# Optimization experiments

Hardware: AMD Instinct MI355X
Metric: run time of the kernel (lower is better)

Reference implementation:

```python
import jax, jax.numpy as jnp
import numpy as np
import math

B, L, DIM = 2, 2048, 2048
N_HEADS, N_KV = 16, 4
HD = DIM // N_HEADS          # 128
N_REP = N_HEADS // N_KV      # 4
THETA = 10000.0


def setup_inputs() -> dict:
    key = jax.random.key(0)
    ks = jax.random.split(key, 6)
    x = jax.random.normal(ks[0], (B, L, DIM), dtype=jnp.float32)
    # rotary phasor freqs_cis = exp(i * t * inv_freq), stored as cos/sin
    inv_freq = 1.0 / (THETA ** (jnp.arange(0, HD, 2, dtype=jnp.float32) / HD))  # [HD//2]
    ang = jnp.arange(L, dtype=jnp.float32)[:, None] * inv_freq[None, :]          # [L, HD//2]
    freqs_cos = jnp.cos(ang)
    freqs_sin = jnp.sin(ang)
    s = 0.02
    wq = jax.random.normal(ks[1], (DIM, DIM), dtype=jnp.float32) * s
    wk = jax.random.normal(ks[2], (N_KV * HD, DIM), dtype=jnp.float32) * s
    wv = jax.random.normal(ks[3], (N_KV * HD, DIM), dtype=jnp.float32) * s
    wo = jax.random.normal(ks[4], (DIM, DIM), dtype=jnp.float32) * s
    return {"x": x, "freqs_cos": freqs_cos, "freqs_sin": freqs_sin,
            "wq": wq, "wk": wk, "wv": wv, "wo": wo}


def _apply_rope(t, cos, sin):
    # t: [B, L, H, HD]; cos/sin: [L, HD//2] -> broadcast [1, L, 1, HD//2]
    tr = t.reshape(*t.shape[:-1], HD // 2, 2)
    t0, t1 = tr[..., 0], tr[..., 1]
    c = cos[None, :, None, :]
    s = sin[None, :, None, :]
    r0 = t0 * c - t1 * s
    r1 = t0 * s + t1 * c
    return jnp.stack([r0, r1], axis=-1).reshape(t.shape)


def reference(x, freqs_cos, freqs_sin, wq, wk, wv, wo):
    Bx, Lx, _ = x.shape
    xq = (x @ wq.T).reshape(Bx, Lx, N_HEADS, HD)
    xk = (x @ wk.T).reshape(Bx, Lx, N_KV, HD)
    xv = (x @ wv.T).reshape(Bx, Lx, N_KV, HD)
    xq = _apply_rope(xq, freqs_cos, freqs_sin)
    xk = _apply_rope(xk, freqs_cos, freqs_sin)
    # repeat_kv (GQA expansion) then [B, H, L, HD]
    keys = jnp.repeat(xk, N_REP, axis=2).transpose(0, 2, 1, 3)
    values = jnp.repeat(xv, N_REP, axis=2).transpose(0, 2, 1, 3)
    q = xq.transpose(0, 2, 1, 3)
    scores = jnp.einsum('bhqd,bhkd->bhqk', q, keys) / math.sqrt(HD)
    mask = jnp.triu(jnp.full((Lx, Lx), -jnp.inf, dtype=scores.dtype), k=1)
    scores = scores + mask[None, None]
    probs = jax.nn.softmax(scores.astype(jnp.float32), axis=-1).astype(q.dtype)
    out = jnp.einsum('bhqk,bhkd->bhqd', probs, values)
    out = out.transpose(0, 2, 1, 3).reshape(Bx, Lx, -1)
    output = out @ wo.T
    return (output, keys, values)
```

## Files before the change

kernel.cpp:

```cpp
#include <hip/hip_runtime.h>
#include <hip/hip_bf16.h>

using bf16x8 = __attribute__((ext_vector_type(8))) short;
using f32x4  = __attribute__((ext_vector_type(4))) float;

__device__ __forceinline__ unsigned short f32_to_bf16(float f) {
  unsigned u = __float_as_uint(f);
  u += 0x7FFFu + ((u >> 16) & 1u);
  return (unsigned short)(u >> 16);
}
__device__ __forceinline__ unsigned pack2(float lo, float hi) {
  __hip_bfloat162 h = __float22bfloat162_rn(make_float2(lo, hi));
  return *reinterpret_cast<unsigned*>(&h);
}
__device__ __forceinline__ void gload_lds16(const void* g, void* l) {
  __builtin_amdgcn_global_load_lds(
      (const __attribute__((address_space(1))) unsigned int*)g,
      (__attribute__((address_space(3))) unsigned int*)l, 16, 0, 0);
}

__global__ void cast_all_kernel(const float* __restrict__ wq, const float* __restrict__ wo,
                                const float* __restrict__ wk, const float* __restrict__ wv,
                                const float* __restrict__ x,
                                unsigned short* __restrict__ WQKV,
                                unsigned short* __restrict__ WO,
                                unsigned short* __restrict__ XBF) {
  int i = blockIdx.x * blockDim.x + threadIdx.x;
  const float4* s; ushort4* d; int j;
  if (i < 1048576)      { s = (const float4*)wq; d = (ushort4*)WQKV;            j = i; }
  else if (i < 2097152) { s = (const float4*)wo; d = (ushort4*)WO;              j = i - 1048576; }
  else if (i < 2359296) { s = (const float4*)wk; d = (ushort4*)WQKV + 1048576;  j = i - 2097152; }
  else if (i < 2621440) { s = (const float4*)wv; d = (ushort4*)WQKV + 1310720;  j = i - 2359296; }
  else                  { s = (const float4*)x;  d = (ushort4*)XBF;             j = i - 2621440; }
  float4 v = s[j];
  ushort4 o;
  o.x = f32_to_bf16(v.x); o.y = f32_to_bf16(v.y);
  o.z = f32_to_bf16(v.z); o.w = f32_to_bf16(v.w);
  d[j] = o;
}

template <int BM>
__global__ __launch_bounds__(512, 2) void gemm256_kernel(
    const unsigned short* __restrict__ A, const unsigned short* __restrict__ Bw,
    float* __restrict__ C, int M, int N, int K) {
  constexpr int ABYTES = BM * 128;
  constexpr int BBYTES = 256 * 128;
  constexpr int BUFB   = ABYTES + BBYTES;
  constexpr int ALOADS = BM / 64;
  constexpr int WROWS  = BM / 32;
  __shared__ __align__(16) char Lsh[2 * BUFB];

  const int tid = threadIdx.x;
  const int wid = tid >> 6, lane = tid & 63;
  const int lr = lane & 15, lg = lane >> 4;
  const int wr = wid >> 2, wc = wid & 3;
  const int bn = blockIdx.x, bm = blockIdx.y;
  const int x0 = lg * 16;

  f32x4 acc[WROWS][4] = {};

  const char* Ag = (const char*)A + (size_t)(bm * BM) * K * 2;
  const char* Bg = (const char*)Bw + (size_t)(bn * 256) * K * 2;

  int aoff[ALOADS], boff[4];
#pragma unroll
  for (int i = 0; i < ALOADS; ++i) {
    int lin = wid * (BM * 16) + i * 1024 + lane * 16;
    int grow = lin >> 7;
    int gcol = (lin & 127) ^ ((grow & 7) << 4);
    aoff[i] = grow * (K * 2) + gcol;
  }
#pragma unroll
  for (int i = 0; i < 4; ++i) {
    int lin = wid * 4096 + i * 1024 + lane * 16;
    int grow = lin >> 7;
    int gcol = (lin & 127) ^ ((grow & 7) << 4);
    boff[i] = grow * (K * 2) + gcol;
  }

  auto stage = [&](int s, int buf) {
    const int kb = s * 128;
    char* Lb = Lsh + buf * BUFB;
#pragma unroll
    for (int i = 0; i < ALOADS; ++i)
      gload_lds16(Ag + aoff[i] + kb, Lb + wid * (BM * 16) + i * 1024);
#pragma unroll
    for (int i = 0; i < 4; ++i)
      gload_lds16(Bg + boff[i] + kb, Lb + ABYTES + wid * 4096 + i * 1024);
  };

  auto kstep = [&](char* Lb) {
    bf16x8 bfr[4][2];
#pragma unroll
    for (int fc = 0; fc < 4; ++fc) {
      const int row = wc * 64 + fc * 16 + lr;
      const int base = ABYTES + row * 128;
      const int sw = (row & 7) << 4;
#pragma unroll
      for (int ks = 0; ks < 2; ++ks)
        bfr[fc][ks] = *reinterpret_cast<const bf16x8*>(Lb + base + ((ks * 64 + x0) ^ sw));
    }
#pragma unroll
    for (int q = 0; q < WROWS / 2; ++q) {
      bf16x8 af[2][2];
#pragma unroll
      for (int t = 0; t < 2; ++t) {
        const int row = wr * (BM / 2) + (2 * q + t) * 16 + lr;
        const int base = row * 128;
        const int sw = (row & 7) << 4;
#pragma unroll
        for (int ks = 0; ks < 2; ++ks)
          af[t][ks] = *reinterpret_cast<const bf16x8*>(Lb + base + ((ks * 64 + x0) ^ sw));
      }
      asm volatile("s_waitcnt lgkmcnt(0)" ::: "memory");
      __builtin_amdgcn_sched_barrier(0);
      __builtin_amdgcn_s_setprio(1);
#pragma unroll
      for (int t = 0; t < 2; ++t)
#pragma unroll
        for (int fc = 0; fc < 4; ++fc) {
          acc[2 * q + t][fc] = __builtin_amdgcn_mfma_f32_16x16x32_bf16(af[t][0], bfr[fc][0], acc[2 * q + t][fc], 0, 0, 0);
          acc[2 * q + t][fc] = __builtin_amdgcn_mfma_f32_16x16x32_bf16(af[t][1], bfr[fc][1], acc[2 * q + t][fc], 0, 0, 0);
        }
      __builtin_amdgcn_s_setprio(0);
    }
  };

  const int NST = K >> 6;
  stage(0, 0);
  for (int it = 0; it < NST / 2; ++it) {
    __builtin_amdgcn_s_barrier();
    stage(2 * it + 1, 1);
    if constexpr (BM == 256) asm volatile("s_waitcnt vmcnt(8)" ::: "memory");
    else                     asm volatile("s_waitcnt vmcnt(6)" ::: "memory");
    __builtin_amdgcn_s_barrier();
    kstep(Lsh);
    __builtin_amdgcn_s_barrier();
    if (it < NST / 2 - 1) {
      stage(2 * it + 2, 0);
      if constexpr (BM == 256) asm volatile("s_waitcnt vmcnt(8)" ::: "memory");
      else                     asm volatile("s_waitcnt vmcnt(6)" ::: "memory");
    } else {
      asm volatile("s_waitcnt vmcnt(0)" ::: "memory");
    }
    __builtin_amdgcn_s_barrier();
    kstep(Lsh + BUFB);
  }

#pragma unroll
  for (int fr = 0; fr < WROWS; ++fr) {
    const int m = bm * BM + wr * (BM / 2) + fr * 16 + lg * 4;
#pragma unroll
    for (int fc = 0; fc < 4; ++fc) {
      const int n = bn * 256 + wc * 64 + fc * 16 + lr;
#pragma unroll
      for (int r = 0; r < 4; ++r)
        C[(size_t)(m + r) * N + n] = acc[fr][fc][r];
    }
  }
}

__global__ void kv_proc_kernel(const float* __restrict__ xqkv, const float* __restrict__ fc,
                               const float* __restrict__ fs, unsigned short* __restrict__ kbf,
                               float* __restrict__ keys, unsigned short* __restrict__ vt,
                               float* __restrict__ values) {
  int bid = blockIdx.x;
  if (bid < 4096) {
    int idx = bid * 256 + threadIdx.x;
    int i = idx & 63;
    int kvh = (idx >> 6) & 3;
    int l = (idx >> 8) & 2047;
    int b = idx >> 19;
    float2 t = reinterpret_cast<const float2*>(xqkv)[(size_t)(b * 2048 + l) * 1536 + 1024 + kvh * 64 + i];
    float c = fc[l * 64 + i], s = fs[l * 64 + i];
    float r0 = t.x * c - t.y * s;
    float r1 = t.x * s + t.y * c;
    int kidx = ((b * 4 + kvh) * 2048 + l) * 64 + i;
    ushort2 o; o.x = f32_to_bf16(r0); o.y = f32_to_bf16(r1);
    reinterpret_cast<ushort2*>(kbf)[kidx] = o;
    float2 f; f.x = r0; f.y = r1;
#pragma unroll
    for (int rep = 0; rep < 4; ++rep) {
      int h = kvh * 4 + rep;
      reinterpret_cast<float2*>(keys)[((b * 16 + h) * 2048 + l) * 64 + i] = f;
    }
  } else {
    int idx = (bid - 4096) * 256 + threadIdx.x;
    int d = idx & 127;
    int kvh = (idx >> 7) & 3;
    int l = (idx >> 9) & 2047;
    int b = idx >> 20;
    float v = xqkv[(size_t)(b * 2048 + l) * 3072 + 2560 + kvh * 128 + d];
#pragma unroll
    for (int rep = 0; rep < 4; ++rep) {
      int h = kvh * 4 + rep;
      values[((size_t)(b * 16 + h) * 2048 + l) * 128 + d] = v;
    }
    vt[((size_t)(b * 4 + kvh) * 128 + d) * 2048 + l] = f32_to_bf16(v);
  }
}

__global__ __launch_bounds__(256) void attn_kernel(
    const float* __restrict__ xq, const float* __restrict__ fc,
    const float* __restrict__ fs, const unsigned short* __restrict__ kbf,
    const unsigned short* __restrict__ vt, unsigned short* __restrict__ obf) {
  __shared__ unsigned short Ks[64 * 128];
  __shared__ unsigned short Vs[128 * 64];
  __shared__ unsigned short Ps[4][2][16 * 72];
  const int tid = threadIdx.x;
  const int w = tid >> 6, lane = tid & 63;
  const int lr = lane & 15, lg = lane >> 4;
  const int bid = blockIdx.x;
  const int qt = 15 - (bid >> 5);
  const int bh = bid & 31;
  const int b = bh >> 4, h = bh & 15, kv = h >> 2;
  const int q0 = qt * 128 + w * 32;
  const float ALPHA = 0.08838834764831845f;
  const int swz = (lr & 7) << 4;

  bf16x8 qf[2][4];
#pragma unroll
  for (int t = 0; t < 2; ++t) {
    const int qrow = q0 + t * 16 + lr;
    const float* xqp = xq + (size_t)(b * 2048 + qrow) * 3072 + h * 128;
    const float* fcp = fc + qrow * 64;
    const float* fsp = fs + qrow * 64;
#pragma unroll
    for (int s = 0; s < 4; ++s) {
      float4 f0 = *reinterpret_cast<const float4*>(xqp + s * 32 + lg * 8);
      float4 f1 = *reinterpret_cast<const float4*>(xqp + s * 32 + lg * 8 + 4);
      float4 c4 = *reinterpret_cast<const float4*>(fcp + s * 16 + lg * 4);
      float4 s4 = *reinterpret_cast<const float4*>(fsp + s * 16 + lg * 4);
      c4.x *= ALPHA; c4.y *= ALPHA; c4.z *= ALPHA; c4.w *= ALPHA;
      s4.x *= ALPHA; s4.y *= ALPHA; s4.z *= ALPHA; s4.w *= ALPHA;
      union { bf16x8 v8; unsigned u[4]; } uu;
      uu.u[0] = pack2(f0.x * c4.x - f0.y * s4.x, f0.x * s4.x + f0.y * c4.x);
      uu.u[1] = pack2(f0.z * c4.y - f0.w * s4.y, f0.z * s4.y + f0.w * c4.y);
      uu.u[2] = pack2(f1.x * c4.z - f1.y * s4.z, f1.x * s4.z + f1.y * c4.z);
      uu.u[3] = pack2(f1.z * c4.w - f1.w * s4.w, f1.z * s4.w + f1.w * c4.w);
      qf[t][s] = uu.v8;
    }
  }

  f32x4 acc[2][8] = {};
  float mrow[2] = {-1e30f, -1e30f}, lsum[2] = {0.f, 0.f};

  const char* kgbase = (const char*)(kbf + (size_t)(b * 4 + kv) * 2048 * 128);
  const char* vgbase = (const char*)(vt + (size_t)(b * 4 + kv) * 128 * 2048);

  const int nblocks = 2 * qt + 2;
  for (int j = 0; j < nblocks; ++j) {
    const int kb = j * 64;
    __syncthreads();
#pragma unroll
    for (int i = 0; i < 4; ++i) {
      int p = w * 4096 + i * 1024 + lane * 16;
      int krow = p >> 8;
      int kcol = (p & 255) ^ ((krow & 7) << 4);
      gload_lds16(kgbase + (size_t)(kb + krow) * 256 + kcol, (char*)Ks + w * 4096 + i * 1024);
      int drow = p >> 7;
      int dcol = (p & 127) ^ ((drow & 7) << 4);
      gload_lds16(vgbase + (size_t)drow * 4096 + (size_t)kb * 2 + dcol, (char*)Vs + w * 4096 + i * 1024);
    }
    __syncthreads();
    if (j == nblocks - 1 && w < 2) continue;
    f32x4 sT[2][4];
#pragma unroll
    for (int c = 0; c < 4; ++c) {
      bf16x8 kf[4];
#pragma unroll
      for (int s = 0; s < 4; ++s)
        kf[s] = *reinterpret_cast<const bf16x8*>((char*)Ks + (((c * 16 + lr) * 256 + s * 64 + lg * 16) ^ swz));
      f32x4 t0 = {0.f, 0.f, 0.f, 0.f}, t1 = {0.f, 0.f, 0.f, 0.f};
#pragma unroll
      for (int s = 0; s < 4; ++s) {
        t0 = __builtin_amdgcn_mfma_f32_16x16x32_bf16(kf[s], qf[0][s], t0, 0, 0, 0);
        t1 = __builtin_amdgcn_mfma_f32_16x16x32_bf16(kf[s], qf[1][s], t1, 0, 0, 0);
      }
      sT[0][c] = t0; sT[1][c] = t1;
    }
#pragma unroll
    for (int t = 0; t < 2; ++t) {
      const int qrow = q0 + t * 16 + lr;
      float x[4][4];
      float mt = -1e30f;
#pragma unroll
      for (int c = 0; c < 4; ++c)
#pragma unroll
        for (int r = 0; r < 4; ++r) {
          int k = kb + c * 16 + lg * 4 + r;
          float v = (k <= qrow) ? sT[t][c][r] : -1e30f;
          x[c][r] = v;
          mt = fmaxf(mt, v);
        }
      mt = fmaxf(mt, __shfl_xor(mt, 16));
      mt = fmaxf(mt, __shfl_xor(mt, 32));
      const bool skip = __all(mt <= mrow[t] + 8.0f);
      float mnew, fac;
      if (skip) {
        mnew = mrow[t];
      } else {
        mnew = fmaxf(mrow[t], mt);
        fac = __expf(mrow[t] - mnew);
        mrow[t] = mnew;
      }
      float rs = 0.f;
      unsigned pw[4][2];
#pragma unroll
      for (int c = 0; c < 4; ++c)
#pragma unroll
        for (int j2 = 0; j2 < 2; ++j2) {
          float p0 = __expf(x[c][2 * j2] - mnew);
          float p1 = __expf(x[c][2 * j2 + 1] - mnew);
          rs += p0 + p1;
          pw[c][j2] = pack2(p0, p1);
        }
      rs += __shfl_xor(rs, 16);
      rs += __shfl_xor(rs, 32);
      if (skip) {
        lsum[t] += rs;
      } else {
        lsum[t] = lsum[t] * fac + rs;
#pragma unroll
        for (int dt = 0; dt < 8; ++dt)
#pragma unroll
          for (int r = 0; r < 4; ++r) acc[t][dt][r] *= fac;
      }
      char* pb = (char*)&Ps[w][t][0];
#pragma unroll
      for (int c = 0; c < 4; ++c)
#pragma unroll
        for (int j2 = 0; j2 < 2; ++j2)
          *reinterpret_cast<unsigned*>(pb + lr * 144 + c * 32 + lg * 8 + j2 * 4) = pw[c][j2];
    }
    asm volatile("s_waitcnt lgkmcnt(0)" ::: "memory");
    __builtin_amdgcn_sched_barrier(0);
    bf16x8 pt[2][2];
#pragma unroll
    for (int t = 0; t < 2; ++t)
#pragma unroll
      for (int kk = 0; kk < 2; ++kk)
        pt[t][kk] = *reinterpret_cast<const bf16x8*>((char*)&Ps[w][t][0] + lr * 144 + kk * 64 + lg * 16);
#pragma unroll
    for (int dt = 0; dt < 8; ++dt) {
      bf16x8 v0 = *reinterpret_cast<const bf16x8*>((char*)Vs + (((dt * 16 + lr) * 128 + lg * 16) ^ swz));
      bf16x8 v1 = *reinterpret_cast<const bf16x8*>((char*)Vs + (((dt * 16 + lr) * 128 + 64 + lg * 16) ^ swz));
      acc[0][dt] = __builtin_amdgcn_mfma_f32_16x16x32_bf16(v0, pt[0][0], acc[0][dt], 0, 0, 0);
      acc[0][dt] = __builtin_amdgcn_mfma_f32_16x16x32_bf16(v1, pt[0][1], acc[0][dt], 0, 0, 0);
      acc[1][dt] = __builtin_amdgcn_mfma_f32_16x16x32_bf16(v0, pt[1][0], acc[1][dt], 0, 0, 0);
      acc[1][dt] = __builtin_amdgcn_mfma_f32_16x16x32_bf16(v1, pt[1][1], acc[1][dt], 0, 0, 0);
    }
  }
#pragma unroll
  for (int t = 0; t < 2; ++t) {
    float inv = 1.0f / lsum[t];
#pragma unroll
    for (int dt = 0; dt < 8; ++dt) {
      ushort4 o;
      o.x = f32_to_bf16(acc[t][dt][0] * inv);
      o.y = f32_to_bf16(acc[t][dt][1] * inv);
      o.z = f32_to_bf16(acc[t][dt][2] * inv);
      o.w = f32_to_bf16(acc[t][dt][3] * inv);
      *reinterpret_cast<ushort4*>(obf + ((size_t)(b * 2048 + q0 + t * 16 + lr)) * 2048 + h * 128 + dt * 16 + lg * 4) = o;
    }
  }
}

extern "C" void kernel_launch(void* const* d_in, const int* in_sizes, int n_in,
                              void* d_out, int out_size, void* d_ws, size_t ws_size,
                              hipStream_t stream) {
  const float* x  = (const float*)d_in[0];
  const float* fc = (const float*)d_in[1];
  const float* fs = (const float*)d_in[2];
  const float* wq = (const float*)d_in[3];
  const float* wk = (const float*)d_in[4];
  const float* wv = (const float*)d_in[5];
  const float* wo = (const float*)d_in[6];

  float* out    = (float*)d_out;
  float* keys   = out + 8388608;
  float* values = out + 16777216;

  char* ws = (char*)d_ws;
  unsigned short* WQKV = (unsigned short*)(ws + 0);
  unsigned short* WO   = (unsigned short*)(ws + 12582912);
  unsigned short* XBF  = (unsigned short*)(ws + 20971520);
  float*          XQKV = (float*)(ws + 37748736);
  unsigned short* KBF  = (unsigned short*)(ws + 88080384);
  unsigned short* VTB  = (unsigned short*)(ws + 92274688);
  unsigned short* ATT  = XBF;

  cast_all_kernel<<<18432, 256, 0, stream>>>(wq, wo, wk, wv, x, WQKV, WO, XBF);

  gemm256_kernel<128><<<dim3(12, 32), 512, 0, stream>>>(XBF, WQKV, XQKV, 4096, 3072, 2048);

  kv_proc_kernel<<<12288, 256, 0, stream>>>(XQKV, fc, fs, KBF, keys, VTB, values);

  attn_kernel<<<512, 256, 0, stream>>>(XQKV, fc, fs, KBF, VTB, ATT);

  gemm256_kernel<128><<<dim3(8, 32), 512, 0, stream>>>(ATT, WO, out, 4096, 2048, 2048);
}
```

Measured before the change: 234.0 us.

## Emit Q projection as bf16 and split KV output; use BM=256 for QKV GEMM

The QKV GEMM epilogue now writes the Q part directly as bf16 into a dense buffer and the K/V part as fp32 into a separate compact buffer, instead of one fp32 XQKV matrix. The attention kernel reads bf16 Q and widens it before applying RoPE, and kv_proc uses the new compact layout. The aim is less epilogue write traffic and less Q read traffic. The QKV GEMM also switches to a 256-row tile with half the blocks in M. Q is now rounded to bf16 before RoPE, which adds a second rounding step.

```diff
diff --git a/kernel.cpp b/kernel.cpp
--- a/kernel.cpp
+++ b/kernel.cpp
@@ -39,10 +39,11 @@
   d[j] = o;
 }
 
-template <int BM>
+template <int BM, int MODE>
 __global__ __launch_bounds__(512, 2) void gemm256_kernel(
     const unsigned short* __restrict__ A, const unsigned short* __restrict__ Bw,
-    float* __restrict__ C, int M, int N, int K) {
+    float* __restrict__ C, unsigned short* __restrict__ qbf_out,
+    float* __restrict__ xkv_out, int M, int N, int K) {
   constexpr int ABYTES = BM * 128;
   constexpr int BBYTES = 256 * 128;
   constexpr int BUFB   = ABYTES + BBYTES;
@@ -147,20 +148,48 @@
     kstep(Lsh + BUFB);
   }
 
-#pragma unroll
-  for (int fr = 0; fr < WROWS; ++fr) {
-    const int m = bm * BM + wr * (BM / 2) + fr * 16 + lg * 4;
-#pragma unroll
-    for (int fc = 0; fc < 4; ++fc) {
-      const int n = bn * 256 + wc * 64 + fc * 16 + lr;
-#pragma unroll
-      for (int r = 0; r < 4; ++r)
-        C[(size_t)(m + r) * N + n] = acc[fr][fc][r];
-    }
-  }
-}
-
-__global__ void kv_proc_kernel(const float* __restrict__ xqkv, const float* __restrict__ fc,
+  if constexpr (MODE == 0) {
+#pragma unroll
+    for (int fr = 0; fr < WROWS; ++fr) {
+      const int m = bm * BM + wr * (BM / 2) + fr * 16 + lg * 4;
+#pragma unroll
+      for (int fc = 0; fc < 4; ++fc) {
+        const int n = bn * 256 + wc * 64 + fc * 16 + lr;
+#pragma unroll
+        for (int r = 0; r < 4; ++r)
+          C[(size_t)(m + r) * N + n] = acc[fr][fc][r];
+      }
+    }
+  } else {
+    if (bn < 8) {
+#pragma unroll
+      for (int fr = 0; fr < WROWS; ++fr) {
+        const int m = bm * BM + wr * (BM / 2) + fr * 16 + lg * 4;
+#pragma unroll
+        for (int fc = 0; fc < 4; ++fc) {
+          const int n = bn * 256 + wc * 64 + fc * 16 + lr;
+#pragma unroll
+          for (int r = 0; r < 4; ++r)
+            qbf_out[(size_t)(m + r) * 2048 + n] = f32_to_bf16(acc[fr][fc][r]);
+        }
+      }
+    } else {
+#pragma unroll
+      for (int fr = 0; fr < WROWS; ++fr) {
+        const int m = bm * BM + wr * (BM / 2) + fr * 16 + lg * 4;
+#pragma unroll
+        for (int fc = 0; fc < 4; ++fc) {
+          const int n = bn * 256 + wc * 64 + fc * 16 + lr - 2048;
+#pragma unroll
+          for (int r = 0; r < 4; ++r)
+            xkv_out[(size_t)(m + r) * 1024 + n] = acc[fr][fc][r];
+        }
+      }
+    }
+  }
+}
+
+__global__ void kv_proc_kernel(const float* __restrict__ xkv, const float* __restrict__ fc,
                                const float* __restrict__ fs, unsigned short* __restrict__ kbf,
                                float* __restrict__ keys, unsigned short* __restrict__ vt,
                                float* __restrict__ values) {
@@ -171,7 +200,7 @@
     int kvh = (idx >> 6) & 3;
     int l = (idx >> 8) & 2047;
     int b = idx >> 19;
-    float2 t = reinterpret_cast<const float2*>(xqkv)[(size_t)(b * 2048 + l) * 1536 + 1024 + kvh * 64 + i];
+    float2 t = reinterpret_cast<const float2*>(xkv)[(size_t)(b * 2048 + l) * 512 + kvh * 64 + i];
     float c = fc[l * 64 + i], s = fs[l * 64 + i];
     float r0 = t.x * c - t.y * s;
     float r1 = t.x * s + t.y * c;
@@ -190,7 +219,7 @@
     int kvh = (idx >> 7) & 3;
     int l = (idx >> 9) & 2047;
     int b = idx >> 20;
-    float v = xqkv[(size_t)(b * 2048 + l) * 3072 + 2560 + kvh * 128 + d];
+    float v = xkv[(size_t)(b * 2048 + l) * 1024 + 512 + kvh * 128 + d];
 #pragma unroll
     for (int rep = 0; rep < 4; ++rep) {
       int h = kvh * 4 + rep;
@@ -201,7 +230,7 @@
 }
 
 __global__ __launch_bounds__(256) void attn_kernel(
-    const float* __restrict__ xq, const float* __restrict__ fc,
+    const unsigned short* __restrict__ qbf, const float* __restrict__ fc,
     const float* __restrict__ fs, const unsigned short* __restrict__ kbf,
     const unsigned short* __restrict__ vt, unsigned short* __restrict__ obf) {
   __shared__ unsigned short Ks[64 * 128];
@@ -222,22 +251,25 @@
 #pragma unroll
   for (int t = 0; t < 2; ++t) {
     const int qrow = q0 + t * 16 + lr;
-    const float* xqp = xq + (size_t)(b * 2048 + qrow) * 3072 + h * 128;
+    const unsigned short* xqp = qbf + (size_t)(b * 2048 + qrow) * 2048 + h * 128;
     const float* fcp = fc + qrow * 64;
     const float* fsp = fs + qrow * 64;
 #pragma unroll
     for (int s = 0; s < 4; ++s) {
-      float4 f0 = *reinterpret_cast<const float4*>(xqp + s * 32 + lg * 8);
-      float4 f1 = *reinterpret_cast<const float4*>(xqp + s * 32 + lg * 8 + 4);
+      union { bf16x8 v8; unsigned short us[8]; } rw;
+      rw.v8 = *reinterpret_cast<const bf16x8*>(xqp + s * 32 + lg * 8);
+      float xv[8];
+#pragma unroll
+      for (int k = 0; k < 8; ++k) xv[k] = __uint_as_float(((unsigned)rw.us[k]) << 16);
       float4 c4 = *reinterpret_cast<const float4*>(fcp + s * 16 + lg * 4);
       float4 s4 = *reinterpret_cast<const float4*>(fsp + s * 16 + lg * 4);
       c4.x *= ALPHA; c4.y *= ALPHA; c4.z *= ALPHA; c4.w *= ALPHA;
       s4.x *= ALPHA; s4.y *= ALPHA; s4.z *= ALPHA; s4.w *= ALPHA;
       union { bf16x8 v8; unsigned u[4]; } uu;
-      uu.u[0] = pack2(f0.x * c4.x - f0.y * s4.x, f0.x * s4.x + f0.y * c4.x);
-      uu.u[1] = pack2(f0.z * c4.y - f0.w * s4.y, f0.z * s4.y + f0.w * c4.y);
-      uu.u[2] = pack2(f1.x * c4.z - f1.y * s4.z, f1.x * s4.z + f1.y * c4.z);
-      uu.u[3] = pack2(f1.z * c4.w - f1.w * s4.w, f1.z * s4.w + f1.w * c4.w);
+      uu.u[0] = pack2(xv[0] * c4.x - xv[1] * s4.x, xv[0] * s4.x + xv[1] * c4.x);
+      uu.u[1] = pack2(xv[2] * c4.y - xv[3] * s4.y, xv[2] * s4.y + xv[3] * c4.y);
+      uu.u[2] = pack2(xv[4] * c4.z - xv[5] * s4.z, xv[4] * s4.z + xv[5] * c4.z);
+      uu.u[3] = pack2(xv[6] * c4.w - xv[7] * s4.w, xv[6] * s4.w + xv[7] * c4.w);
       qf[t][s] = uu.v8;
     }
   }
@@ -385,18 +417,21 @@
   unsigned short* WQKV = (unsigned short*)(ws + 0);
   unsigned short* WO   = (unsigned short*)(ws + 12582912);
   unsigned short* XBF  = (unsigned short*)(ws + 20971520);
-  float*          XQKV = (float*)(ws + 37748736);
+  unsigned short* QBF  = (unsigned short*)(ws + 37748736);
+  float*          XKV  = (float*)(ws + 54525952);
   unsigned short* KBF  = (unsigned short*)(ws + 88080384);
   unsigned short* VTB  = (unsigned short*)(ws + 92274688);
   unsigned short* ATT  = XBF;
 
   cast_all_kernel<<<18432, 256, 0, stream>>>(wq, wo, wk, wv, x, WQKV, WO, XBF);
 
-  gemm256_kernel<128><<<dim3(12, 32), 512, 0, stream>>>(XBF, WQKV, XQKV, 4096, 3072, 2048);
-
-  kv_proc_kernel<<<12288, 256, 0, stream>>>(XQKV, fc, fs, KBF, keys, VTB, values);
-
-  attn_kernel<<<512, 256, 0, stream>>>(XQKV, fc, fs, KBF, VTB, ATT);
-
-  gemm256_kernel<128><<<dim3(8, 32), 512, 0, stream>>>(ATT, WO, out, 4096, 2048, 2048);
-}
+  gemm256_kernel<256, 1><<<dim3(12, 16), 512, 0, stream>>>(
+      XBF, WQKV, nullptr, QBF, XKV, 4096, 3072, 2048);
+
+  kv_proc_kernel<<<12288, 256, 0, stream>>>(XKV, fc, fs, KBF, keys, VTB, values);
+
+  attn_kernel<<<512, 256, 0, stream>>>(QBF, fc, fs, KBF, VTB, ATT);
+
+  gemm256_kernel<128, 0><<<dim3(8, 32), 512, 0, stream>>>(
+      ATT, WO, out, nullptr, nullptr, 4096, 2048, 2048);
+}
```

After: 223.1 us. 1.05x faster.
